# Optimization experiments

Hardware: AMD Instinct MI355X
Metric: run time of the kernel (lower is better)

## Reference

```python
import jax, jax.numpy as jnp
import numpy as np
import math

B, T, C = 4, 2048, 1024
NH, D = 16, 64


def setup_inputs() -> dict:
    key = jax.random.key(0)
    ks = jax.random.split(key, 7)
    s = 0.02
    return {
        "x": jax.random.normal(ks[0], (B, T, C), dtype=jnp.float32),
        "W_attn": jax.random.normal(ks[1], (C, 3 * C), dtype=jnp.float32) * s,
        "b_attn": jax.random.normal(ks[2], (3 * C,), dtype=jnp.float32) * s,
        "W_proj": jax.random.normal(ks[3], (C, C), dtype=jnp.float32) * s,
        "b_proj": jax.random.normal(ks[4], (C,), dtype=jnp.float32) * s,
        # bQ/bK emulate mean_Q + std_Q*randn (resampled biases), broadcast over heads
        "bQ": 0.5 + 0.1 * jax.random.normal(ks[5], (NH, D), dtype=jnp.float32),
        "bK": 0.3 + 0.1 * jax.random.normal(ks[6], (NH, D), dtype=jnp.float32),
    }


def reference(x, W_attn, b_attn, W_proj, b_proj, bQ, bK):
    b, t, c = x.shape
    nh, d = bQ.shape
    qkv = x @ W_attn + b_attn                       # [B,T,3C]
    q, k, v = jnp.split(qkv, 3, axis=2)
    # [B,T,C] -> [B,nh,T,d]
    q = q.reshape(b, t, nh, d).transpose(0, 2, 1, 3)
    k = k.reshape(b, t, nh, d).transpose(0, 2, 1, 3)
    v = v.reshape(b, t, nh, d).transpose(0, 2, 1, 3)
    q = q + bQ[None, :, None, :]
    k = k + bK[None, :, None, :]
    scores = jnp.einsum('bhqd,bhkd->bhqk', q, k) / math.sqrt(d)
    causal = jnp.tril(jnp.ones((t, t), dtype=bool))
    scores = jnp.where(causal[None, None], scores, jnp.finfo(scores.dtype).min)
    att = jax.nn.softmax(scores, axis=-1)
    y = jnp.einsum('bhqk,bhkd->bhqd', att, v)       # [B,nh,T,d]
    y = y.transpose(0, 2, 1, 3).reshape(b, t, c)
    out = y @ W_proj + b_proj
    return (out, bQ)
```

## Files before the change

kernel.cpp:

```cpp
#include <hip/hip_runtime.h>
#include <hip/hip_bf16.h>

#define B_  4
#define T_  2048
#define C_  1024
#define NH_ 16
#define D_  64
#define BH_ (B_*NH_)
#define M_  (B_*T_)

typedef __attribute__((ext_vector_type(8))) short short8;
typedef __attribute__((ext_vector_type(4))) short short4v;
typedef __attribute__((ext_vector_type(4))) float f32x4;

#define SC2 0.18033688011112043f

__device__ __forceinline__ ushort f2bf(float f) {
    unsigned u = __float_as_uint(f);
    u += 0x7FFF + ((u >> 16) & 1);
    return (ushort)(u >> 16);
}

__device__ __forceinline__ unsigned cvtpk(float lo, float hi) {
    unsigned r;
    asm("v_cvt_pk_bf16_f32 %0, %1, %2" : "=v"(r) : "v"(lo), "v"(hi));
    return r;
}

__device__ __forceinline__ void gload16(const void* g, void* lds) {
    __builtin_amdgcn_global_load_lds(
        (const __attribute__((address_space(1))) void*)g,
        (__attribute__((address_space(3))) void*)lds, 16, 0, 0);
}

__global__ __launch_bounds__(256) void convert_x_kernel(
    const float* __restrict__ in, ushort* __restrict__ out, int n8)
{
    const int stride = gridDim.x * 256;
    for (int idx = blockIdx.x * 256 + threadIdx.x; idx < n8; idx += stride) {
        const float* p = in + (size_t)idx * 8;
        f32x4 a = *(const f32x4*)p;
        f32x4 b = *(const f32x4*)(p + 4);
        union { short8 v; ushort u[8]; } pk;
        #pragma unroll
        for (int j = 0; j < 4; ++j) { pk.u[j] = f2bf(a[j]); pk.u[4+j] = f2bf(b[j]); }
        *(short8*)&out[(size_t)idx * 8] = pk.v;
    }
}

__global__ __launch_bounds__(256) void transpose_w_kernel(
    const float* __restrict__ in, ushort* __restrict__ out, int K, int N)
{
    __shared__ float t[64][65];
    const int tid = threadIdx.x;
    const int n0 = blockIdx.x * 64;
    const int k0 = blockIdx.y * 64;
    #pragma unroll
    for (int it = 0; it < 16; ++it) {
        const int kr = it*4 + (tid >> 6);
        t[kr][tid & 63] = in[(size_t)(k0 + kr) * N + n0 + (tid & 63)];
    }
    __syncthreads();
    const int nr8 = tid >> 3;
    const int kc0 = (tid & 7) * 8;
    #pragma unroll
    for (int j = 0; j < 2; ++j) {
        const int nr = j*32 + nr8;
        union { short8 v; ushort u[8]; } pk;
        #pragma unroll
        for (int e = 0; e < 8; ++e) pk.u[e] = f2bf(t[kc0 + e][nr]);
        *(short8*)&out[(size_t)(n0 + nr) * K + k0 + kc0] = pk.v;
    }
}

template<int MODE>
__global__ __launch_bounds__(256) void gemm128_kernel(
    const ushort* __restrict__ A, const ushort* __restrict__ Bt,
    const float* __restrict__ b_attn, const float* __restrict__ bQv,
    const float* __restrict__ bKv,
    ushort* __restrict__ Qb, ushort* __restrict__ Kb, ushort* __restrict__ Vt,
    float* __restrict__ outp, const float* __restrict__ b_proj,
    int K, int N)
{
    __shared__ ushort As[3][128*32];
    __shared__ ushort Bs[3][128*32];

    const int tid  = threadIdx.x;
    const int lane = tid & 63;
    const int w    = tid >> 6;
    const int wr   = w >> 1, wc = w & 1;
    const int l16  = lane & 15, lg = lane >> 4;
    const int m0   = blockIdx.x * 128, n0 = blockIdx.y * 128;

    const int srow = lane >> 2;
    const int scol = (lane & 3) * 8;
    const ushort* aS = A  + (size_t)(m0 + w*32 + srow) * K + scol;
    const ushort* bS = Bt + (size_t)(n0 + w*32 + srow) * K + scol;

    f32x4 acc[4][4] = {};

    const int NT = K >> 5;

    #define STAGE(tk, bi)                                              \
        do {                                                           \
            const int kn_ = (tk) * 32;                                 \
            gload16(aS + kn_,                As[bi] + w*1024);         \
            gload16(aS + (size_t)16*K + kn_, As[bi] + w*1024 + 512);   \
            gload16(bS + kn_,                Bs[bi] + w*1024);         \
            gload16(bS + (size_t)16*K + kn_, Bs[bi] + w*1024 + 512);   \
        } while (0)

    STAGE(0, 0);
    STAGE(1, 1);
    asm volatile("s_waitcnt vmcnt(4)" ::: "memory");
    __builtin_amdgcn_s_barrier();

    for (int t = 0; t < NT; ++t) {
        const int cur = t % 3;
        if (t + 2 < NT)
            STAGE(t + 2, (t + 2) % 3);

        short8 af[4], bf[4];
        #pragma unroll
        for (int i = 0; i < 4; ++i) {
            af[i] = *(const short8*)&As[cur][(wr*64 + i*16 + l16)*32 + lg*8];
            bf[i] = *(const short8*)&Bs[cur][(wc*64 + i*16 + l16)*32 + lg*8];
        }
        #pragma unroll
        for (int mi = 0; mi < 4; ++mi)
            #pragma unroll
            for (int ni = 0; ni < 4; ++ni)
                acc[mi][ni] = __builtin_amdgcn_mfma_f32_16x16x32_bf16(
                    af[mi], bf[ni], acc[mi][ni], 0, 0, 0);

        if (t + 1 < NT) {
            if (t + 2 < NT)
                asm volatile("s_waitcnt vmcnt(4)" ::: "memory");
            else
                asm volatile("s_waitcnt vmcnt(0)" ::: "memory");
            __builtin_amdgcn_s_barrier();
        }
    }
    #undef STAGE

    #pragma unroll
    for (int ni = 0; ni < 4; ++ni) {
        const int n = n0 + wc*64 + ni*16 + l16;
        if constexpr (MODE == 0) {
            const int sec = n >> 10;
            const int nn  = n & 1023;
            const int h = nn >> 6, d = nn & 63;
            const float ba = b_attn[n];
            #pragma unroll
            for (int mi = 0; mi < 4; ++mi) {
                #pragma unroll
                for (int r = 0; r < 4; ++r) {
                    const int m = m0 + wr*64 + mi*16 + lg*4 + r;
                    const int b = m >> 11, t = m & 2047;
                    float v = acc[mi][ni][r] + ba;
                    if (sec == 0) {
                        v = (v + bQv[nn]) * SC2;
                        Qb[((size_t)(b*NH_ + h)*T_ + t)*D_ + d] = f2bf(v);
                    } else if (sec == 1) {
                        v += bKv[nn];
                        Kb[((size_t)(b*NH_ + h)*T_ + t)*D_ + d] = f2bf(v);
                    } else {
                        Vt[((size_t)(b*NH_ + h)*D_ + d)*T_ + t] = f2bf(v);
                    }
                }
            }
        } else {
            const float bp = b_proj[n];
            #pragma unroll
            for (int mi = 0; mi < 4; ++mi)
                #pragma unroll
                for (int r = 0; r < 4; ++r) {
                    const int m = m0 + wr*64 + mi*16 + lg*4 + r;
                    outp[(size_t)m * N + n] = acc[mi][ni][r] + bp;
                }
        }
    }
}

__global__ __launch_bounds__(256, 5) void attn_kernel(
    const ushort* __restrict__ Qb, const ushort* __restrict__ Kb,
    const ushort* __restrict__ Vt, ushort* __restrict__ y)
{
    __shared__ char lds[2][16384];

    const int tid  = threadIdx.x;
    const int lane = tid & 63;
    const int w    = tid >> 6;
    const int l16  = lane & 15, lg = lane >> 4;
    const int bid  = blockIdx.x;
    const int xcd  = bid & 7;
    const int idx  = bid >> 3;
    const int bh   = (xcd << 3) | (idx & 7);
    const int p    = 31 - (idx >> 3);
    const int b    = bh >> 4, h = bh & 15;
    const size_t kvb = (size_t)bh * T_ * D_;
    const size_t vtb = (size_t)bh * D_ * T_;

    int srow[2], scol[2];
    #pragma unroll
    for (int i = 0; i < 2; ++i) {
        const int l = w*2048 + i*1024 + lane*16;
        const int r = l >> 7;
        const int c = (l & 127) ^ ((r & 7) << 4);
        srow[i] = r; scol[i] = c >> 1;
    }

    const f32x4 z4 = {0.f, 0.f, 0.f, 0.f};

    const int qw = p * 64 + w * 16;

    short8 qf[2];
    #pragma unroll
    for (int c = 0; c < 2; ++c)
        qf[c] = *(const short8*)(Qb + kvb +
                    (size_t)(qw + l16)*D_ + c*32 + lg*8);

    f32x4 o[4] = {};
    float mrow = -1e30f;
    float lrow = 0.f;
    const int nt = p + 1;

    #pragma unroll
    for (int i = 0; i < 2; ++i) {
        gload16(Kb + kvb + (size_t)srow[i]*D_ + scol[i],
                &lds[0][w*2048 + i*1024]);
        gload16(Vt + vtb + (size_t)srow[i]*T_ + scol[i],
                &lds[0][8192 + w*2048 + i*1024]);
    }

    #pragma unroll 1
    for (int t = 0; t < nt; ++t) {
        const int kb = t * 64;
        if (t + 1 < nt) {
            char* Lb = lds[(t + 1) & 1];
            const int kb1 = kb + 64;
            #pragma unroll
            for (int i = 0; i < 2; ++i) {
                gload16(Kb + kvb + (size_t)(kb1 + srow[i])*D_ + scol[i],
                        Lb + w*2048 + i*1024);
                gload16(Vt + vtb + (size_t)srow[i]*T_ + kb1 + scol[i],
                        Lb + 8192 + w*2048 + i*1024);
            }
            asm volatile("s_waitcnt vmcnt(4)" ::: "memory");
        } else {
            asm volatile("s_waitcnt vmcnt(0)" ::: "memory");
        }
        __builtin_amdgcn_s_barrier();

        {
            const char* Lk = lds[t & 1];
            const char* Lv = lds[t & 1] + 8192;

            f32x4 s[4];
            #pragma unroll
            for (int t4 = 0; t4 < 4; ++t4) {
                const int r = t4*16 + l16;
                const int m = (r & 7) << 4;
                const short8 kc0 = *(const short8*)(Lk + r*128 + (( lg*16     ) ^ m));
                const short8 kc1 = *(const short8*)(Lk + r*128 + ((64 + lg*16 ) ^ m));
                s[t4] = __builtin_amdgcn_mfma_f32_16x16x32_bf16(kc0, qf[0], z4,    0, 0, 0);
                s[t4] = __builtin_amdgcn_mfma_f32_16x16x32_bf16(kc1, qf[1], s[t4], 0, 0, 0);
            }

            const bool full = (kb + 63 <= qw);
            float x[4][4];
            #pragma unroll
            for (int t4 = 0; t4 < 4; ++t4)
                #pragma unroll
                for (int r = 0; r < 4; ++r) {
                    float v = s[t4][r];
                    if (!full)
                        v = (kb + t4*16 + lg*4 + r <= qw + l16) ? v : -1e30f;
                    x[t4][r] = v;
                }
            float vm0 = fmaxf(fmaxf(x[0][0], x[0][1]), fmaxf(x[0][2], x[0][3]));
            float vm1 = fmaxf(fmaxf(x[1][0], x[1][1]), fmaxf(x[1][2], x[1][3]));
            float vm2 = fmaxf(fmaxf(x[2][0], x[2][1]), fmaxf(x[2][2], x[2][3]));
            float vm3 = fmaxf(fmaxf(x[3][0], x[3][1]), fmaxf(x[3][2], x[3][3]));
            float vm  = fmaxf(fmaxf(vm0, vm1), fmaxf(vm2, vm3));
            vm = fmaxf(vm, __shfl_xor(vm, 16, 64));
            vm = fmaxf(vm, __shfl_xor(vm, 32, 64));
            const float mn = fmaxf(mrow, vm);
            float rs = 0.f;
            #pragma unroll
            for (int t4 = 0; t4 < 4; ++t4)
                #pragma unroll
                for (int r = 0; r < 4; ++r) {
                    const float pe = __builtin_amdgcn_exp2f(x[t4][r] - mn);
                    x[t4][r] = pe;
                    rs += pe;
                }
            rs += __shfl_xor(rs, 16, 64);
            rs += __shfl_xor(rs, 32, 64);
            if (__all(vm <= mrow)) {
                lrow += rs;
            } else {
                const float al = __builtin_amdgcn_exp2f(mrow - mn);
                lrow = lrow*al + rs;
                #pragma unroll
                for (int cb = 0; cb < 4; ++cb)
                    #pragma unroll
                    for (int r = 0; r < 4; ++r)
                        o[cb][r] *= al;
            }
            mrow = mn;

            union { unsigned u[4]; short8 v; } p0, p1;
            p0.u[0] = cvtpk(x[0][0], x[0][1]);
            p0.u[1] = cvtpk(x[0][2], x[0][3]);
            p0.u[2] = cvtpk(x[1][0], x[1][1]);
            p0.u[3] = cvtpk(x[1][2], x[1][3]);
            p1.u[0] = cvtpk(x[2][0], x[2][1]);
            p1.u[1] = cvtpk(x[2][2], x[2][3]);
            p1.u[2] = cvtpk(x[3][0], x[3][1]);
            p1.u[3] = cvtpk(x[3][2], x[3][3]);

            #pragma unroll
            for (int cb = 0; cb < 4; ++cb) {
                const int d = cb*16 + l16;
                const int mv = (d & 7) << 4;
                const char* vb = Lv + d*128;
                union { short8 v; short4v hh[2]; } v0, v1;
                v0.hh[0] = *(const short4v*)(vb + ((lg*8     ) ^ mv));
                v0.hh[1] = *(const short4v*)(vb + ((lg*8 + 32) ^ mv));
                v1.hh[0] = *(const short4v*)(vb + ((lg*8 + 64) ^ mv));
                v1.hh[1] = *(const short4v*)(vb + ((lg*8 + 96) ^ mv));
                o[cb] = __builtin_amdgcn_mfma_f32_16x16x32_bf16(v0.v, p0.v, o[cb], 0, 0, 0);
                o[cb] = __builtin_amdgcn_mfma_f32_16x16x32_bf16(v1.v, p1.v, o[cb], 0, 0, 0);
            }
        }
        __builtin_amdgcn_s_barrier();
    }

    {
        const float inv = 1.0f / lrow;
        const int q = qw + l16;
        ushort* yr = y + ((size_t)b*T_ + q)*C_ + h*D_ + lg*4;
        #pragma unroll
        for (int cb = 0; cb < 4; ++cb) {
            union { unsigned u[2]; short4v v; } st;
            st.u[0] = cvtpk(o[cb][0]*inv, o[cb][1]*inv);
            st.u[1] = cvtpk(o[cb][2]*inv, o[cb][3]*inv);
            *(short4v*)(yr + cb*16) = st.v;
        }
    }
}

__global__ void copy_bq_kernel(const float* __restrict__ bQ, float* __restrict__ dst) {
    const int i = blockIdx.x * 256 + threadIdx.x;
    if (i < NH_ * D_) dst[i] = bQ[i];
}

extern "C" void kernel_launch(void* const* d_in, const int* in_sizes, int n_in,
                              void* d_out, int out_size, void* d_ws, size_t ws_size,
                              hipStream_t stream)
{
    const float* x      = (const float*)d_in[0];
    const float* W_attn = (const float*)d_in[1];
    const float* b_attn = (const float*)d_in[2];
    const float* W_proj = (const float*)d_in[3];
    const float* b_proj = (const float*)d_in[4];
    const float* bQ     = (const float*)d_in[5];
    const float* bK     = (const float*)d_in[6];
    float* out = (float*)d_out;

    const size_t HE = (size_t)BH_ * T_ * D_;
    ushort* Qb = (ushort*)d_ws;
    ushort* Kb = Qb + HE;
    ushort* Vt = Kb + HE;
    ushort* y  = Vt + HE;
    ushort* Wpt = (ushort*)d_ws;

    ushort* Xb  = (ushort*)d_out;
    ushort* Wat = (ushort*)d_out + (size_t)M_ * C_;

    convert_x_kernel<<<2048, 256, 0, stream>>>(x, Xb, M_*C_/8);
    transpose_w_kernel<<<dim3(3*C_/64, C_/64), 256, 0, stream>>>(W_attn, Wat, C_, 3*C_);

    gemm128_kernel<0><<<dim3(M_/128, 3*C_/128), 256, 0, stream>>>(
        Xb, Wat, b_attn, bQ, bK, Qb, Kb, Vt, nullptr, nullptr, C_, 3*C_);

    attn_kernel<<<2048, 256, 0, stream>>>(Qb, Kb, Vt, y);

    transpose_w_kernel<<<dim3(C_/64, C_/64), 256, 0, stream>>>(W_proj, Wpt, C_, C_);

    gemm128_kernel<1><<<dim3(M_/128, C_/128), 256, 0, stream>>>(
        y, Wpt, nullptr, nullptr, nullptr, nullptr, nullptr, nullptr,
        out, b_proj, C_, C_);

    copy_bq_kernel<<<(NH_*D_ + 255)/256, 256, 0, stream>>>(
        bQ, out + (size_t)M_ * C_);
}
```

Baseline: 208.7 us.

## Fuse prepass kernels, remap GEMM blocks per XCD, stage V transpose through LDS

Merges the x conversion, W_attn transpose and bQ copy into one prepass launch, which removes two kernel launches. Both GEMMs switch to a 1D grid whose block index is remapped so that blocks sharing an XCD work on nearby M tiles, aiming for better L2 reuse. In the QKV GEMM epilogue, V tiles are transposed through LDS so Vt is written with coalesced 16-byte stores instead of scattered 2-byte stores. The cost is an extra pair of barriers and LDS traffic in the V-section blocks.

Measured after the change: 200.0 us. 1.04x faster.

```diff
diff --git a/kernel.cpp b/kernel.cpp
--- a/kernel.cpp
+++ b/kernel.cpp
@@ -33,18 +33,50 @@
         (__attribute__((address_space(3))) void*)lds, 16, 0, 0);
 }
 
-__global__ __launch_bounds__(256) void convert_x_kernel(
-    const float* __restrict__ in, ushort* __restrict__ out, int n8)
+__global__ __launch_bounds__(256) void prepass_kernel(
+    const float* __restrict__ x, ushort* __restrict__ Xb,
+    const float* __restrict__ Wa, ushort* __restrict__ Wat,
+    const float* __restrict__ bQ, float* __restrict__ bqDst)
 {
-    const int stride = gridDim.x * 256;
-    for (int idx = blockIdx.x * 256 + threadIdx.x; idx < n8; idx += stride) {
-        const float* p = in + (size_t)idx * 8;
-        f32x4 a = *(const f32x4*)p;
-        f32x4 b = *(const f32x4*)(p + 4);
-        union { short8 v; ushort u[8]; } pk;
-        #pragma unroll
-        for (int j = 0; j < 4; ++j) { pk.u[j] = f2bf(a[j]); pk.u[4+j] = f2bf(b[j]); }
-        *(short8*)&out[(size_t)idx * 8] = pk.v;
+    __shared__ float t[64][65];
+    const int bid = blockIdx.x;
+    const int tid = threadIdx.x;
+
+    if (bid < 2048) {
+        const int n8 = M_*C_/8;
+        const int stride = 2048 * 256;
+        for (int idx = bid*256 + tid; idx < n8; idx += stride) {
+            const float* p = x + (size_t)idx * 8;
+            f32x4 a = *(const f32x4*)p;
+            f32x4 b = *(const f32x4*)(p + 4);
+            union { short8 v; ushort u[8]; } pk;
+            #pragma unroll
+            for (int j = 0; j < 4; ++j) { pk.u[j] = f2bf(a[j]); pk.u[4+j] = f2bf(b[j]); }
+            *(short8*)&Xb[(size_t)idx * 8] = pk.v;
+        }
+    } else if (bid < 2816) {
+        const int tb = bid - 2048;
+        const int n0 = (tb % 48) * 64;
+        const int k0 = (tb / 48) * 64;
+        const int K = C_, N = 3*C_;
+        #pragma unroll
+        for (int it = 0; it < 16; ++it) {
+            const int kr = it*4 + (tid >> 6);
+            t[kr][tid & 63] = Wa[(size_t)(k0 + kr) * N + n0 + (tid & 63)];
+        }
+        __syncthreads();
+        const int nr8 = tid >> 3;
+        const int kc0 = (tid & 7) * 8;
+        #pragma unroll
+        for (int j = 0; j < 2; ++j) {
+            const int nr = j*32 + nr8;
+            union { short8 v; ushort u[8]; } pk;
+            #pragma unroll
+            for (int e = 0; e < 8; ++e) pk.u[e] = f2bf(t[kc0 + e][nr]);
+            *(short8*)&Wat[(size_t)(n0 + nr) * K + k0 + kc0] = pk.v;
+        }
+    } else {
+        for (int i = tid; i < NH_*D_; i += 256) bqDst[i] = bQ[i];
     }
 }
 
@@ -82,15 +114,19 @@
     float* __restrict__ outp, const float* __restrict__ b_proj,
     int K, int N)
 {
-    __shared__ ushort As[3][128*32];
-    __shared__ ushort Bs[3][128*32];
+    __shared__ ushort SH[24576];
 
     const int tid  = threadIdx.x;
     const int lane = tid & 63;
     const int w    = tid >> 6;
     const int wr   = w >> 1, wc = w & 1;
     const int l16  = lane & 15, lg = lane >> 4;
-    const int m0   = blockIdx.x * 128, n0 = blockIdx.y * 128;
+
+    const int bid = blockIdx.x;
+    const int xcd = bid & 7;
+    const int idx = bid >> 3;
+    const int m0  = (xcd*8 + (idx & 7)) * 128;
+    const int n0  = (idx >> 3) * 128;
 
     const int srow = lane >> 2;
     const int scol = (lane & 3) * 8;
@@ -101,13 +137,13 @@
 
     const int NT = K >> 5;
 
-    #define STAGE(tk, bi)                                              \
-        do {                                                           \
-            const int kn_ = (tk) * 32;                                 \
-            gload16(aS + kn_,                As[bi] + w*1024);         \
-            gload16(aS + (size_t)16*K + kn_, As[bi] + w*1024 + 512);   \
-            gload16(bS + kn_,                Bs[bi] + w*1024);         \
-            gload16(bS + (size_t)16*K + kn_, Bs[bi] + w*1024 + 512);   \
+    #define STAGE(tk, bi)                                                     \
+        do {                                                                  \
+            const int kn_ = (tk) * 32;                                        \
+            gload16(aS + kn_,                SH + (bi)*4096 + w*1024);        \
+            gload16(aS + (size_t)16*K + kn_, SH + (bi)*4096 + w*1024 + 512);  \
+            gload16(bS + kn_,                SH + 12288 + (bi)*4096 + w*1024);\
+            gload16(bS + (size_t)16*K + kn_, SH + 12288 + (bi)*4096 + w*1024 + 512);\
         } while (0)
 
     STAGE(0, 0);
@@ -123,8 +159,8 @@
         short8 af[4], bf[4];
         #pragma unroll
         for (int i = 0; i < 4; ++i) {
-            af[i] = *(const short8*)&As[cur][(wr*64 + i*16 + l16)*32 + lg*8];
-            bf[i] = *(const short8*)&Bs[cur][(wc*64 + i*16 + l16)*32 + lg*8];
+            af[i] = *(const short8*)&SH[cur*4096 + (wr*64 + i*16 + l16)*32 + lg*8];
+            bf[i] = *(const short8*)&SH[12288 + cur*4096 + (wc*64 + i*16 + l16)*32 + lg*8];
         }
         #pragma unroll
         for (int mi = 0; mi < 4; ++mi)
@@ -143,33 +179,64 @@
     }
     #undef STAGE
 
-    #pragma unroll
-    for (int ni = 0; ni < 4; ++ni) {
-        const int n = n0 + wc*64 + ni*16 + l16;
-        if constexpr (MODE == 0) {
-            const int sec = n >> 10;
-            const int nn  = n & 1023;
-            const int h = nn >> 6, d = nn & 63;
-            const float ba = b_attn[n];
-            #pragma unroll
-            for (int mi = 0; mi < 4; ++mi) {
-                #pragma unroll
-                for (int r = 0; r < 4; ++r) {
-                    const int m = m0 + wr*64 + mi*16 + lg*4 + r;
-                    const int b = m >> 11, t = m & 2047;
-                    float v = acc[mi][ni][r] + ba;
-                    if (sec == 0) {
-                        v = (v + bQv[nn]) * SC2;
-                        Qb[((size_t)(b*NH_ + h)*T_ + t)*D_ + d] = f2bf(v);
-                    } else if (sec == 1) {
-                        v += bKv[nn];
-                        Kb[((size_t)(b*NH_ + h)*T_ + t)*D_ + d] = f2bf(v);
-                    } else {
-                        Vt[((size_t)(b*NH_ + h)*D_ + d)*T_ + t] = f2bf(v);
+    if constexpr (MODE == 0) {
+        if (n0 >= 2048) {
+            __syncthreads();
+            ushort* TL = SH;
+            #pragma unroll
+            for (int ni = 0; ni < 4; ++ni) {
+                const int nl = wc*64 + ni*16 + l16;
+                const float ba = b_attn[n0 + nl];
+                #pragma unroll
+                for (int mi = 0; mi < 4; ++mi)
+                    #pragma unroll
+                    for (int r = 0; r < 4; ++r) {
+                        const int ml = wr*64 + mi*16 + lg*4 + r;
+                        TL[nl*136 + ml] = f2bf(acc[mi][ni][r] + ba);
+                    }
+            }
+            __syncthreads();
+            const int bblk = m0 >> 11;
+            const int tblk = m0 & 2047;
+            const int h0   = (n0 & 1023) >> 6;
+            #pragma unroll
+            for (int it = 0; it < 8; ++it) {
+                const int row = w*32 + it*4 + (lane >> 4);
+                const int d   = row & 63;
+                const int h   = h0 + (row >> 6);
+                const short8 v = *(const short8*)&TL[row*136 + (lane & 15)*8];
+                *(short8*)(Vt + ((size_t)(bblk*NH_ + h)*D_ + d)*T_ + tblk + (lane & 15)*8) = v;
+            }
+        } else {
+            #pragma unroll
+            for (int ni = 0; ni < 4; ++ni) {
+                const int n = n0 + wc*64 + ni*16 + l16;
+                const int sec = n >> 10;
+                const int nn  = n & 1023;
+                const int h = nn >> 6, d = nn & 63;
+                const float ba = b_attn[n];
+                #pragma unroll
+                for (int mi = 0; mi < 4; ++mi) {
+                    #pragma unroll
+                    for (int r = 0; r < 4; ++r) {
+                        const int m = m0 + wr*64 + mi*16 + lg*4 + r;
+                        const int b = m >> 11, t = m & 2047;
+                        float v = acc[mi][ni][r] + ba;
+                        if (sec == 0) {
+                            v = (v + bQv[nn]) * SC2;
+                            Qb[((size_t)(b*NH_ + h)*T_ + t)*D_ + d] = f2bf(v);
+                        } else {
+                            v += bKv[nn];
+                            Kb[((size_t)(b*NH_ + h)*T_ + t)*D_ + d] = f2bf(v);
+                        }
                     }
                 }
             }
-        } else {
+        }
+    } else {
+        #pragma unroll
+        for (int ni = 0; ni < 4; ++ni) {
+            const int n = n0 + wc*64 + ni*16 + l16;
             const float bp = b_proj[n];
             #pragma unroll
             for (int mi = 0; mi < 4; ++mi)
@@ -351,11 +418,6 @@
     }
 }
 
-__global__ void copy_bq_kernel(const float* __restrict__ bQ, float* __restrict__ dst) {
-    const int i = blockIdx.x * 256 + threadIdx.x;
-    if (i < NH_ * D_) dst[i] = bQ[i];
-}
-
 extern "C" void kernel_launch(void* const* d_in, const int* in_sizes, int n_in,
                               void* d_out, int out_size, void* d_ws, size_t ws_size,
                               hipStream_t stream)
@@ -379,20 +441,17 @@
     ushort* Xb  = (ushort*)d_out;
     ushort* Wat = (ushort*)d_out + (size_t)M_ * C_;
 
-    convert_x_kernel<<<2048, 256, 0, stream>>>(x, Xb, M_*C_/8);
-    transpose_w_kernel<<<dim3(3*C_/64, C_/64), 256, 0, stream>>>(W_attn, Wat, C_, 3*C_);
-
-    gemm128_kernel<0><<<dim3(M_/128, 3*C_/128), 256, 0, stream>>>(
+    prepass_kernel<<<2817, 256, 0, stream>>>(x, Xb, W_attn, Wat,
+                                             bQ, out + (size_t)M_ * C_);
+
+    gemm128_kernel<0><<<1536, 256, 0, stream>>>(
         Xb, Wat, b_attn, bQ, bK, Qb, Kb, Vt, nullptr, nullptr, C_, 3*C_);
 
     attn_kernel<<<2048, 256, 0, stream>>>(Qb, Kb, Vt, y);
 
     transpose_w_kernel<<<dim3(C_/64, C_/64), 256, 0, stream>>>(W_proj, Wpt, C_, C_);
 
-    gemm128_kernel<1><<<dim3(M_/128, C_/128), 256, 0, stream>>>(
+    gemm128_kernel<1><<<512, 256, 0, stream>>>(
         y, Wpt, nullptr, nullptr, nullptr, nullptr, nullptr, nullptr,
         out, b_proj, C_, C_);
-
-    copy_bq_kernel<<<(NH_*D_ + 255)/256, 256, 0, stream>>>(
-        bQ, out + (size_t)M_ * C_);
-}
+}
```
